# Kernel optimization log

Hardware: AMD Instinct MI355X
Metric: run time of the kernel (lower is better)

## Reference

```python
import jax, jax.numpy as jnp
import numpy as np


def setup_inputs() -> dict:
    key = jax.random.key(0)
    B, L, H, D = 4, 4096, 8, 64
    sample_k = int(np.ceil(np.log(L)))  # factor=1 -> U_part = ceil(ln L_K) = 9
    k1, k2, k3, k4 = jax.random.split(key, 4)
    return {
        "queries": jax.random.normal(k1, (B, L, H, D), jnp.float32),
        "keys": jax.random.normal(k2, (B, L, H, D), jnp.float32),
        "values": jax.random.normal(k3, (B, L, H, D), jnp.float32),
        "index_sample": jax.random.randint(k4, (L, sample_k), 0, L),
    }


def _prob_attention(Q, K, V, index_sample):
    # Q, K, V: [B, H, L, D]
    B, H, L_K, D = K.shape
    L_Q = Q.shape[2]
    u = min(int(np.ceil(np.log(L_Q))), L_Q)  # n_top (static)

    # --- _prob_QK: sampled scores, sparsity measure M, top-u queries ---
    # gather sampled keys per query position: [B, H, L_Q, sample_k, D]
    K_sample = K[:, :, index_sample, :]
    QK_sample = jnp.einsum('bhld,bhlsd->bhls', Q, K_sample)  # [B,H,L_Q,S]
    M = QK_sample.max(axis=-1) - QK_sample.sum(axis=-1) / L_K  # [B,H,L_Q]
    _, M_top = jax.lax.top_k(M, u)  # [B,H,u] indices of top queries

    Q_reduce = jnp.take_along_axis(Q, M_top[..., None], axis=2)  # [B,H,u,D]
    scale = 1.0 / jnp.sqrt(jnp.asarray(D, Q.dtype))
    scores = jnp.einsum('bhud,bhkd->bhuk', Q_reduce, K) * scale  # [B,H,u,L_K]

    # --- initial context (mask_flag=False): mean of V over keys ---
    context = jnp.broadcast_to(V.mean(axis=2, keepdims=True), (B, H, L_Q, D))

    # --- update context at the top-u query positions ---
    attn = jax.nn.softmax(scores, axis=-1)  # [B,H,u,L_K]
    ctx_top = jnp.einsum('bhuk,bhkd->bhud', attn, V)  # [B,H,u,D]
    b_idx = jnp.arange(B)[:, None, None]
    h_idx = jnp.arange(H)[None, :, None]
    context = context.at[b_idx, h_idx, M_top].set(ctx_top)
    return context, attn


def reference(queries, keys, values, index_sample):
    # inputs: [B, L, H, D] -> internal [B, H, L, D]
    Q = queries.transpose(0, 2, 1, 3)
    K = keys.transpose(0, 2, 1, 3)
    V = values.transpose(0, 2, 1, 3)
    context, attn = _prob_attention(Q, K, V, index_sample)
    return context.transpose(0, 2, 1, 3), attn
```

## Files before the change

kernel.cpp:

```cpp
#include <hip/hip_runtime.h>
#include <math.h>

#define B_ 4
#define L_ 4096
#define H_ 8
#define D_ 64
#define S_ 9
#define U_ 9
#define VC_ 64
#define NC_ 32
#define CC_ 16
#define TKC_ 8

#define VMBLK_ 256
#define MBLK_ 4096
#define FILLBLK_ 8192

__device__ __forceinline__ float dot4(const float4& a, const float4& b) {
    return a.x * b.x + a.y * b.y + a.z * b.z + a.w * b.w;
}

__global__ void __launch_bounds__(256, 4)
kernel_M_vmean(const float* __restrict__ Q, const float* __restrict__ K,
               const int* __restrict__ idx, float* __restrict__ M,
               const float* __restrict__ V, float* __restrict__ vpart) {
    if (blockIdx.x < VMBLK_) {
        int blk = blockIdx.x;
        int c = blk & (VC_ - 1), b = blk >> 6;
        int col = threadIdx.x & 127;
        int lp  = threadIdx.x >> 7;
        const int CHUNK = L_ / VC_;
        const float4* base = (const float4*)(V + (size_t)b * L_ * H_ * D_);
        float4 acc = make_float4(0.f, 0.f, 0.f, 0.f);
        for (int l = c * CHUNK + lp; l < (c + 1) * CHUNK; l += 2) {
            float4 v = base[(size_t)l * 128 + col];
            acc.x += v.x; acc.y += v.y; acc.z += v.z; acc.w += v.w;
        }
        __shared__ float4 red[256];
        red[threadIdx.x] = acc;
        __syncthreads();
        if (lp == 0) {
            float4 o = red[threadIdx.x + 128];
            acc.x += o.x; acc.y += o.y; acc.z += o.z; acc.w += o.w;
            ((float4*)vpart)[(size_t)blk * 128 + col] = acc;
        }
        return;
    }
    int t = threadIdx.x;
    int wid = t >> 6, lane = t & 63;
    int w = ((blockIdx.x - VMBLK_) << 2) + wid;
    int b = __builtin_amdgcn_readfirstlane(w >> 12);
    int l = __builtin_amdgcn_readfirstlane(w & (L_ - 1));

    int ki[S_];
#pragma unroll
    for (int s = 0; s < S_; ++s) ki[s] = idx[l * S_ + s];

    const float4* qb = (const float4*)(Q + (size_t)(b * L_ + l) * (H_ * D_));
    float4 q0 = qb[2 * lane];
    float4 q1 = qb[2 * lane + 1];

    const float* Kb = K + (size_t)b * L_ * (H_ * D_);

    float4 ka[S_], kc[S_];
#pragma unroll
    for (int s = 0; s < S_; ++s) {
        const float4* kp = (const float4*)(Kb + (size_t)ki[s] * (H_ * D_));
        ka[s] = kp[2 * lane];
        kc[s] = kp[2 * lane + 1];
    }

    float mx = -INFINITY, sm = 0.0f;
#pragma unroll
    for (int s = 0; s < S_; ++s) {
        float d = dot4(q0, ka[s]) + dot4(q1, kc[s]);
        d += __shfl_xor(d, 1);
        d += __shfl_xor(d, 2);
        d += __shfl_xor(d, 4);
        mx = fmaxf(mx, d);
        sm += d;
    }
    if ((lane & 7) == 0) {
        int h = lane >> 3;
        M[((size_t)(b * H_ + h) << 12) + l] = mx - sm * (1.0f / (float)L_);
    }
}

#define CSWAP(a, b)                                                          \
    if (v[b] > v[a] || (v[b] == v[a] && id[b] < id[a])) {                    \
        float tv = v[a]; v[a] = v[b]; v[b] = tv;                             \
        int ti = id[a]; id[a] = id[b]; id[b] = ti;                           \
    }

__global__ void kernel_topk1(const float* __restrict__ M,
                             float* __restrict__ cand_v, int* __restrict__ cand_i) {
    int bh = blockIdx.x >> 3;
    int chunk = blockIdx.x & (TKC_ - 1);
    int lane = threadIdx.x;
    const float* Ms = M + ((size_t)bh << 12);

    float v[8]; int id[8];
#pragma unroll
    for (int c = 0; c < 8; ++c) {
        int gi = chunk * 512 + lane + 64 * c;
        v[c] = Ms[gi]; id[c] = gi;
    }
    CSWAP(0,1) CSWAP(2,3) CSWAP(4,5) CSWAP(6,7)
    CSWAP(0,2) CSWAP(1,3) CSWAP(4,6) CSWAP(5,7)
    CSWAP(1,2) CSWAP(5,6)
    CSWAP(0,4) CSWAP(1,5) CSWAP(2,6) CSWAP(3,7)
    CSWAP(2,4) CSWAP(3,5)
    CSWAP(1,2) CSWAP(3,4) CSWAP(5,6)

    float* cv = cand_v + (size_t)blockIdx.x * U_;
    int*   ci = cand_i + (size_t)blockIdx.x * U_;
#pragma unroll
    for (int r = 0; r < U_; ++r) {
        float bv = v[0]; int bi = id[0];
#pragma unroll
        for (int off = 1; off < 64; off <<= 1) {
            float ov = __shfl_xor(bv, off);
            int   oi = __shfl_xor(bi, off);
            if (ov > bv || (ov == bv && oi < bi)) { bv = ov; bi = oi; }
        }
        if (lane == 0) { cv[r] = bv; ci[r] = bi; }
        if (id[0] == bi) {
#pragma unroll
            for (int c = 0; c < 7; ++c) { v[c] = v[c+1]; id[c] = id[c+1]; }
            v[7] = -INFINITY; id[7] = 0x7fffffff;
        }
    }
}

__global__ void kernel_small(const float* __restrict__ cand_v, const int* __restrict__ cand_i,
                             int* __restrict__ Mtop, const float* __restrict__ vpart,
                             float* __restrict__ vmean) {
    if (blockIdx.x >= 32) {
        int bh = blockIdx.x - 32;
        int h = bh & (H_ - 1), b = bh >> 3;
        int d = threadIdx.x;
        float s = 0.0f;
        for (int c = 0; c < VC_; ++c)
            s += vpart[(size_t)(b * VC_ + c) * (H_ * D_) + h * D_ + d];
        vmean[bh * D_ + d] = s * (1.0f / (float)L_);
        return;
    }
    int bh = blockIdx.x;
    int lane = threadIdx.x;
    const float* cv = cand_v + (size_t)bh * (TKC_ * U_);
    const int*   ci = cand_i + (size_t)bh * (TKC_ * U_);

    float v[2]; int id[2];
    v[0] = cv[lane]; id[0] = ci[lane];
    if (lane < TKC_ * U_ - 64) { v[1] = cv[64 + lane]; id[1] = ci[64 + lane]; }
    else { v[1] = -INFINITY; id[1] = 0x7fffffff; }
    CSWAP(0,1)

#pragma unroll
    for (int r = 0; r < U_; ++r) {
        float bv = v[0]; int bi = id[0];
#pragma unroll
        for (int off = 1; off < 64; off <<= 1) {
            float ov = __shfl_xor(bv, off);
            int   oi = __shfl_xor(bi, off);
            if (ov > bv || (ov == bv && oi < bi)) { bv = ov; bi = oi; }
        }
        if (lane == 0) Mtop[bh * U_ + r] = bi;
        if (id[0] == bi) { v[0] = v[1]; id[0] = id[1]; v[1] = -INFINITY; id[1] = 0x7fffffff; }
    }
}

__global__ void kernel_fill_scores(float* __restrict__ out, const float* __restrict__ vmean,
                                   const float* __restrict__ Q, const float* __restrict__ K,
                                   const int* __restrict__ Mtop, float* __restrict__ raw) {
    if (blockIdx.x < FILLBLK_) {
        int i = blockIdx.x * 256 + threadIdx.x;
        int d4 = i & 15;
        int h  = (i >> 4) & (H_ - 1);
        int b  = i >> (4 + 3 + 12);
        ((float4*)out)[i] = ((const float4*)vmean)[(b * H_ + h) * 16 + d4];
        return;
    }
    int n = blockIdx.x - FILLBLK_;
    int x = n & 7, m = n >> 3;
    int chunk = m & (NC_ - 1);
    int bh = (m >> 5) * 8 + x;
    int h = bh & (H_ - 1), b = bh >> 3;
    int k0 = chunk * (L_ / NC_);

    __shared__ float qs[U_][D_];
    int t = threadIdx.x;
    if (t < 144) {
        int u = t / 16, c = t & 15;
        int l = Mtop[bh * U_ + u];
        ((float4*)qs[u])[c] =
            ((const float4*)(Q + (size_t)((b * L_ + l) * H_ + h) * D_))[c];
    }
    __syncthreads();

    int j = t & 3, g = t >> 2;
#pragma unroll
    for (int kk = 0; kk < 2; ++kk) {
        int k = k0 + g + 64 * kk;
        const float4* kb = (const float4*)(K + (size_t)((b * L_ + k) * H_ + h) * D_);
        float4 kv[4];
#pragma unroll
        for (int c = 0; c < 4; ++c) kv[c] = kb[j + 4 * c];
#pragma unroll
        for (int u = 0; u < U_; ++u) {
            float acc = 0.0f;
#pragma unroll
            for (int c = 0; c < 4; ++c)
                acc += dot4(((const float4*)qs[u])[j + 4 * c], kv[c]);
            acc += __shfl_xor(acc, 1);
            acc += __shfl_xor(acc, 2);
            if (j == 0) raw[((size_t)bh * U_ + u) * L_ + k] = acc * 0.125f;
        }
    }
}

__global__ void kernel_softmax(float* __restrict__ attn) {
    int row = blockIdx.x;
    float4* a = (float4*)(attn + (size_t)row * L_);
    int t = threadIdx.x;

    float4 v[4];
    float mx = -INFINITY;
#pragma unroll
    for (int i = 0; i < 4; ++i) {
        v[i] = a[t + 256 * i];
        mx = fmaxf(mx, fmaxf(fmaxf(v[i].x, v[i].y), fmaxf(v[i].z, v[i].w)));
    }
    __shared__ float red[256];
    __shared__ float bmax, bsum;
    red[t] = mx;
    __syncthreads();
    for (int off = 128; off > 0; off >>= 1) {
        if (t < off) red[t] = fmaxf(red[t], red[t + off]);
        __syncthreads();
    }
    if (t == 0) bmax = red[0];
    __syncthreads();

    float mm = bmax, sum = 0.0f;
#pragma unroll
    for (int i = 0; i < 4; ++i) {
        v[i].x = expf(v[i].x - mm); v[i].y = expf(v[i].y - mm);
        v[i].z = expf(v[i].z - mm); v[i].w = expf(v[i].w - mm);
        sum += v[i].x + v[i].y + v[i].z + v[i].w;
    }
    red[t] = sum;
    __syncthreads();
    for (int off = 128; off > 0; off >>= 1) {
        if (t < off) red[t] += red[t + off];
        __syncthreads();
    }
    if (t == 0) bsum = red[0];
    __syncthreads();

    float inv = 1.0f / bsum;
#pragma unroll
    for (int i = 0; i < 4; ++i) {
        v[i].x *= inv; v[i].y *= inv; v[i].z *= inv; v[i].w *= inv;
        a[t + 256 * i] = v[i];
    }
}

__global__ void kernel_ctxf(const float* __restrict__ attn, const float* __restrict__ V,
                            float* __restrict__ cpart) {
    int n = blockIdx.x;
    int x = n & 7, m = n >> 3;
    int chunk = m & (CC_ - 1);
    int bh = (m >> 4) * 8 + x;
    int h = bh & (H_ - 1), b = bh >> 3;
    int k0 = chunk * (L_ / CC_);

    int t = threadIdx.x;
    int g = t >> 6, lane = t & 63;
    int kl = lane >> 4, d4 = lane & 15;
    const float* abase = attn + (size_t)bh * U_ * L_;

    float4 acc[U_];
#pragma unroll
    for (int u = 0; u < U_; ++u) acc[u] = make_float4(0.f, 0.f, 0.f, 0.f);

    for (int i = 0; i < 16; ++i) {
        int k = k0 + (g * 4 + kl) + 16 * i;
        float4 vv = *(const float4*)(V + (size_t)((b * L_ + k) * H_ + h) * D_ + 4 * d4);
        float av[U_];
#pragma unroll
        for (int u = 0; u < U_; ++u) av[u] = abase[(size_t)u * L_ + k];
#pragma unroll
        for (int u = 0; u < U_; ++u) {
            acc[u].x += av[u] * vv.x; acc[u].y += av[u] * vv.y;
            acc[u].z += av[u] * vv.z; acc[u].w += av[u] * vv.w;
        }
    }
#pragma unroll
    for (int u = 0; u < U_; ++u) {
        acc[u].x += __shfl_xor(acc[u].x, 16); acc[u].y += __shfl_xor(acc[u].y, 16);
        acc[u].z += __shfl_xor(acc[u].z, 16); acc[u].w += __shfl_xor(acc[u].w, 16);
        acc[u].x += __shfl_xor(acc[u].x, 32); acc[u].y += __shfl_xor(acc[u].y, 32);
        acc[u].z += __shfl_xor(acc[u].z, 32); acc[u].w += __shfl_xor(acc[u].w, 32);
    }
    __shared__ float4 red[U_][4][16];
    if (kl == 0) {
#pragma unroll
        for (int u = 0; u < U_; ++u) red[u][g][d4] = acc[u];
    }
    __syncthreads();
    if (t < U_ * 16) {
        int u = t >> 4, dd = t & 15;
        float4 s0 = red[u][0][dd], s1 = red[u][1][dd];
        float4 s2 = red[u][2][dd], s3 = red[u][3][dd];
        float4 s = make_float4(s0.x + s1.x + s2.x + s3.x, s0.y + s1.y + s2.y + s3.y,
                               s0.z + s1.z + s2.z + s3.z, s0.w + s1.w + s2.w + s3.w);
        ((float4*)cpart)[((size_t)(bh * CC_ + chunk) * U_ + u) * 16 + dd] = s;
    }
}

__global__ void kernel_ctx2(const float* __restrict__ cpart, const int* __restrict__ Mtop,
                            float* __restrict__ out) {
    int row = blockIdx.x;
    int u = row % U_, bh = row / U_;
    int h = bh & (H_ - 1), b = bh >> 3;
    int d = threadIdx.x;
    float s = 0.0f;
#pragma unroll
    for (int c = 0; c < CC_; ++c)
        s += cpart[((size_t)(bh * CC_ + c) * U_ + u) * 64 + d];
    int l = Mtop[bh * U_ + u];
    out[(size_t)((b * L_ + l) * H_ + h) * D_ + d] = s;
}

extern "C" void kernel_launch(void* const* d_in, const int* in_sizes, int n_in,
                              void* d_out, int out_size, void* d_ws, size_t ws_size,
                              hipStream_t stream) {
    const float* Q   = (const float*)d_in[0];
    const float* K   = (const float*)d_in[1];
    const float* V   = (const float*)d_in[2];
    const int*   idx = (const int*)d_in[3];

    float* ctx_out  = (float*)d_out;
    float* attn_out = (float*)d_out + (size_t)B_ * L_ * H_ * D_;

    float* M      = (float*)d_ws;
    float* vpart  = M + (size_t)B_ * H_ * L_;
    float* vmean  = vpart + (size_t)B_ * VC_ * H_ * D_;
    float* cpart  = vmean + B_ * H_ * D_;
    float* cand_v = cpart + (size_t)32 * CC_ * U_ * 64;
    int*   cand_i = (int*)(cand_v + 32 * TKC_ * U_);
    int*   Mtop   = cand_i + 32 * TKC_ * U_;

    kernel_M_vmean<<<VMBLK_ + MBLK_, 256, 0, stream>>>(Q, K, idx, M, V, vpart);
    kernel_topk1<<<B_ * H_ * TKC_, 64, 0, stream>>>(M, cand_v, cand_i);
    kernel_small<<<64, 64, 0, stream>>>(cand_v, cand_i, Mtop, vpart, vmean);
    kernel_fill_scores<<<FILLBLK_ + 32 * NC_, 256, 0, stream>>>(ctx_out, vmean, Q, K, Mtop, attn_out);
    kernel_softmax<<<B_ * H_ * U_, 256, 0, stream>>>(attn_out);
    kernel_ctxf<<<32 * CC_, 256, 0, stream>>>(attn_out, V, cpart);
    kernel_ctx2<<<B_ * H_ * U_, 64, 0, stream>>>(cpart, Mtop, ctx_out);
}
```

Measured before the change: 220.1 us.

## Restructure score kernel to process all heads per key row with staged writes

The scores section of the fill kernel is remapped so that each block covers one batch and a 32-key chunk across all 8 heads. A wavefront reads whole contiguous K rows (all heads × D) with a register prefetch of the next row, and the top-u query vectors are kept in registers instead of shared memory. Per-head dot products are reduced with three xor shuffles, staged in a padded shared tile, then written back as coalesced runs along the key dimension. This targets strided, poorly coalesced K reads and scattered single-lane stores, at the cost of higher register pressure (18 float4 query registers plus prefetch) under a launch-bounds hint.

```diff
diff --git a/kernel.cpp b/kernel.cpp
--- a/kernel.cpp
+++ b/kernel.cpp
@@ -8,9 +8,10 @@
 #define S_ 9
 #define U_ 9
 #define VC_ 64
-#define NC_ 32
 #define CC_ 16
 #define TKC_ 8
+#define KCH_ 32
+#define SCB_ (B_ * (L_ / KCH_))
 
 #define VMBLK_ 256
 #define MBLK_ 4096
@@ -170,9 +171,10 @@
     }
 }
 
-__global__ void kernel_fill_scores(float* __restrict__ out, const float* __restrict__ vmean,
-                                   const float* __restrict__ Q, const float* __restrict__ K,
-                                   const int* __restrict__ Mtop, float* __restrict__ raw) {
+__global__ void __launch_bounds__(256, 4)
+kernel_fill_scores(float* __restrict__ out, const float* __restrict__ vmean,
+                   const float* __restrict__ Q, const float* __restrict__ K,
+                   const int* __restrict__ Mtop, float* __restrict__ raw) {
     if (blockIdx.x < FILLBLK_) {
         int i = blockIdx.x * 256 + threadIdx.x;
         int d4 = i & 15;
@@ -182,40 +184,63 @@
         return;
     }
     int n = blockIdx.x - FILLBLK_;
-    int x = n & 7, m = n >> 3;
-    int chunk = m & (NC_ - 1);
-    int bh = (m >> 5) * 8 + x;
-    int h = bh & (H_ - 1), b = bh >> 3;
-    int k0 = chunk * (L_ / NC_);
-
-    __shared__ float qs[U_][D_];
+    int b = n >> 7;
+    int chunk = n & 127;
+    int k0 = chunk * KCH_;
+
     int t = threadIdx.x;
-    if (t < 144) {
-        int u = t / 16, c = t & 15;
-        int l = Mtop[bh * U_ + u];
-        ((float4*)qs[u])[c] =
-            ((const float4*)(Q + (size_t)((b * L_ + l) * H_ + h) * D_))[c];
-    }
-    __syncthreads();
-
-    int j = t & 3, g = t >> 2;
-#pragma unroll
-    for (int kk = 0; kk < 2; ++kk) {
-        int k = k0 + g + 64 * kk;
-        const float4* kb = (const float4*)(K + (size_t)((b * L_ + k) * H_ + h) * D_);
-        float4 kv[4];
-#pragma unroll
-        for (int c = 0; c < 4; ++c) kv[c] = kb[j + 4 * c];
+    int w = t >> 6, lane = t & 63;
+    int h = lane >> 3, dq = lane & 7;
+    int bh = b * H_ + h;
+
+    float4 q0[U_], q1[U_];
+#pragma unroll
+    for (int u = 0; u < U_; ++u) {
+        int mi = Mtop[bh * U_ + u];
+        const float4* qp = (const float4*)(Q + (size_t)((b * L_ + mi) * H_ + h) * D_);
+        q0[u] = qp[2 * dq];
+        q1[u] = qp[2 * dq + 1];
+    }
+
+    __shared__ float sc[H_][U_][KCH_ + 1];
+
+    const float* Kb = K + (size_t)b * L_ * (H_ * D_);
+    const float4* kp = (const float4*)(Kb + (size_t)(k0 + w * 8) * (H_ * D_));
+    float4 kv0 = kp[2 * lane], kv1 = kp[2 * lane + 1];
+#pragma unroll
+    for (int i = 0; i < 8; ++i) {
+        int kloc = w * 8 + i;
+        float4 nv0, nv1;
+        if (i < 7) {
+            const float4* np = (const float4*)(Kb + (size_t)(k0 + kloc + 1) * (H_ * D_));
+            nv0 = np[2 * lane]; nv1 = np[2 * lane + 1];
+        }
+        float p[U_];
 #pragma unroll
         for (int u = 0; u < U_; ++u) {
-            float acc = 0.0f;
-#pragma unroll
-            for (int c = 0; c < 4; ++c)
-                acc += dot4(((const float4*)qs[u])[j + 4 * c], kv[c]);
-            acc += __shfl_xor(acc, 1);
-            acc += __shfl_xor(acc, 2);
-            if (j == 0) raw[((size_t)bh * U_ + u) * L_ + k] = acc * 0.125f;
-        }
+            float d = dot4(q0[u], kv0) + dot4(q1[u], kv1);
+            d += __shfl_xor(d, 1);
+            d += __shfl_xor(d, 2);
+            d += __shfl_xor(d, 4);
+            p[u] = d;
+        }
+        float val = p[0];
+#pragma unroll
+        for (int u = 1; u < 8; ++u) val = (dq == u) ? p[u] : val;
+        sc[h][dq][kloc] = val;
+        if (dq == 0) sc[h][8][kloc] = p[8];
+        kv0 = nv0; kv1 = nv1;
+    }
+    __syncthreads();
+
+#pragma unroll
+    for (int r = 0; r < 9; ++r) {
+        int j = r * 256 + t;
+        int kloc = j & 31;
+        int hu = j >> 5;
+        int h2 = hu / U_, u2 = hu - h2 * U_;
+        raw[((size_t)(b * H_ + h2) * U_ + u2) * L_ + k0 + kloc] =
+            sc[h2][u2][kloc] * 0.125f;
     }
 }
 
@@ -355,7 +380,7 @@
     kernel_M_vmean<<<VMBLK_ + MBLK_, 256, 0, stream>>>(Q, K, idx, M, V, vpart);
     kernel_topk1<<<B_ * H_ * TKC_, 64, 0, stream>>>(M, cand_v, cand_i);
     kernel_small<<<64, 64, 0, stream>>>(cand_v, cand_i, Mtop, vpart, vmean);
-    kernel_fill_scores<<<FILLBLK_ + 32 * NC_, 256, 0, stream>>>(ctx_out, vmean, Q, K, Mtop, attn_out);
+    kernel_fill_scores<<<FILLBLK_ + SCB_, 256, 0, stream>>>(ctx_out, vmean, Q, K, Mtop, attn_out);
     kernel_softmax<<<B_ * H_ * U_, 256, 0, stream>>>(attn_out);
     kernel_ctxf<<<32 * CC_, 256, 0, stream>>>(attn_out, V, cpart);
     kernel_ctx2<<<B_ * H_ * U_, 64, 0, stream>>>(cpart, Mtop, ctx_out);
```

Result: faster. 195.7 us (-11.1%).
